# Kernel tuning notes

Measured on AMD Instinct MI355X. Metric: run time of the kernel, lower is better.

Reference implementation:

```python
import jax, jax.numpy as jnp
import numpy as np

N = 50000      # nodes
E = 1600000    # edges
D = 128        # input_dim
H = 128        # hidden_dim
C = 10         # n_class
G = 512        # number of graphs (max(idx)+1)
LRELU_ALPHA = 0.05
BN_EPS = 1e-5


def setup_inputs() -> dict:
    key = jax.random.key(0)
    ks = jax.random.split(key, 10)
    x_in = jax.random.normal(ks[0], (N, D), dtype=jnp.float32)
    edge_index = jax.random.randint(ks[1], (2, E), 0, N, dtype=jnp.int32)
    idx = jnp.sort(jax.random.randint(ks[2], (N,), 0, G, dtype=jnp.int32))

    def lin(k, shape, fan_in):
        return jax.random.normal(k, shape, dtype=jnp.float32) / np.sqrt(fan_in).astype(np.float32)

    fc_w = lin(ks[3], (H, D), D)        # GATLayer.fc weight
    a1 = lin(ks[4], (H,), 2 * H)        # a weight, src half
    a2 = lin(ks[5], (H,), 2 * H)        # a weight, dst half
    fc1_w = lin(ks[6], (H, H), H)
    fc1_b = jnp.zeros((H,), jnp.float32)
    fc2_w = lin(ks[7], (C, H), H)
    fc2_b = jnp.zeros((C,), jnp.float32)
    gamma = jnp.ones((H,), jnp.float32)  # BatchNorm weight
    beta = jnp.zeros((H,), jnp.float32)  # BatchNorm bias
    return {"x_in": x_in, "edge_index": edge_index, "idx": idx,
            "fc_w": fc_w, "a1": a1, "a2": a2,
            "fc1_w": fc1_w, "fc1_b": fc1_b, "fc2_w": fc2_w, "fc2_b": fc2_b,
            "gamma": gamma, "beta": beta}


def reference(x_in, edge_index, idx, fc_w, a1, a2, fc1_w, fc1_b, fc2_w, fc2_b, gamma, beta):
    # input standardization (torch.std is unbiased -> ddof=1)
    x = (x_in - jnp.mean(x_in)) / jnp.std(x_in, ddof=1)

    # ---- GAT layer ----
    z = x @ fc_w.T                              # [N, H]
    src, dst = edge_index[0], edge_index[1]
    # a([z_src ; z_dst]) == z_src@a1 + z_dst@a2  (avoids materializing [E, 2H])
    s1 = z @ a1                                  # [N]
    s2 = z @ a2                                  # [N]
    e = s1[src] + s2[dst]                        # [E]
    e = jnp.where(e >= 0, e, LRELU_ALPHA * e)    # LeakyReLU(0.05)
    h = jnp.exp(e)
    h_sum = jax.ops.segment_sum(h, src, num_segments=N)   # edge-softmax denom per src row
    alpha = h / h_sum[src]                       # [E]
    # sparse.mm(adj_att, z): out[src] += alpha * z[dst]
    out = jax.ops.segment_sum(alpha[:, None] * z[dst], src, num_segments=N)  # [N, H]

    x = jax.nn.relu(out)
    # dropout: identity (eval / deterministic reference)

    # sum pooling per graph
    pooled = jax.ops.segment_sum(x, idx, num_segments=G)   # [G, H]

    # BatchNorm1d (training-mode batch statistics, biased var)
    mu = jnp.mean(pooled, axis=0)
    var = jnp.var(pooled, axis=0)
    xb = (pooled - mu) / jnp.sqrt(var + BN_EPS) * gamma + beta

    x = jax.nn.relu(xb @ fc1_w.T + fc1_b)
    logits = x @ fc2_w.T + fc2_b
    return jax.nn.log_softmax(logits, axis=1)
```

## Files before the change

### kernel.cpp

```cpp
#include <hip/hip_runtime.h>

#define NN 50000
#define NE 1600000
#define DD 128
#define HH 128
#define CC 10
#define GG 512
#define LRELU_A 0.05f
#define BN_EPS 1e-5f

#define TT 256
#define EPT (NE / TT)
#define NB 196
#define NPB 256
#define KNODE 8
#define STB 1024

typedef unsigned int u32;
typedef unsigned short u16;
typedef unsigned char u8;

__device__ __forceinline__ u16 f2bf(float f) {
    u32 u = __float_as_uint(f);
    u32 r = u + 0x7FFFu + ((u >> 16) & 1u);
    return (u16)(r >> 16);
}

__global__ __launch_bounds__(256) void k_front(const int* __restrict__ src,
                                               const float* __restrict__ x,
                                               u16* __restrict__ cnt_b,
                                               u8* __restrict__ rank_e,
                                               float* __restrict__ pooled,
                                               double* __restrict__ pst) {
    __shared__ u32 h[NB];
    __shared__ double ls[4], lss[4];
    int bid = blockIdx.x, tid = threadIdx.x;
    if (bid < TT) {
        for (int i = tid; i < NB; i += 256) h[i] = 0;
        pooled[bid * 256 + tid] = 0.f;
        __syncthreads();
        int e0 = bid * EPT;
        for (int i = tid; i < EPT; i += 256) {
            int b = src[e0 + i] >> 8;
            u32 old = atomicAdd(&h[b], 1u);
            rank_e[e0 + i] = (u8)old;
        }
        __syncthreads();
        for (int i = tid; i < NB; i += 256) cnt_b[bid * NB + i] = (u16)h[i];
    } else {
        int sb = bid - TT;
        const int M4 = NN * DD / 4;
        double s = 0.0, ss = 0.0;
        for (int i = sb * 256 + tid; i < M4; i += STB * 256) {
            float4 v = reinterpret_cast<const float4*>(x)[i];
            s  += (double)v.x + (double)v.y + (double)v.z + (double)v.w;
            ss += (double)v.x * v.x + (double)v.y * v.y + (double)v.z * v.z +
                  (double)v.w * v.w;
        }
        for (int d = 32; d; d >>= 1) { s += __shfl_down(s, d); ss += __shfl_down(ss, d); }
        int lane = tid & 63, w = tid >> 6;
        if (lane == 0) { ls[w] = s; lss[w] = ss; }
        __syncthreads();
        if (tid == 0) {
            pst[2 * sb]     = ls[0] + ls[1] + ls[2] + ls[3];
            pst[2 * sb + 1] = lss[0] + lss[1] + lss[2] + lss[3];
        }
    }
}

__global__ __launch_bounds__(256) void k_mid(const u16* __restrict__ cnt_b,
                                             const double* __restrict__ pst,
                                             const float* __restrict__ fc_w,
                                             u16* __restrict__ rel_b,
                                             int* __restrict__ base_b,
                                             float* __restrict__ wsum,
                                             float* __restrict__ musig,
                                             float* __restrict__ wt) {
    int t = threadIdx.x;
    if (blockIdx.x == 0) {
        __shared__ int sm[256];
        int b = t;
        int run = 0;
        if (b < NB) {
            for (int tt = 0; tt < TT; ++tt) {
                int c = cnt_b[tt * NB + b];
                rel_b[tt * NB + b] = (u16)run;
                run += c;
            }
        }
        sm[b] = (b < NB) ? run : 0;
        __syncthreads();
        int v = sm[b];
        for (int d = 1; d < 256; d <<= 1) {
            int x = 0;
            if (b >= d) x = sm[b - d];
            __syncthreads();
            if (b >= d) sm[b] += x;
            __syncthreads();
        }
        if (b < NB) base_b[b] = sm[b] - v;
        if (b == NB - 1) base_b[NB] = sm[b];
    } else {
        __shared__ double rs[256], rss[256];
        double s  = pst[2 * t] + pst[2 * (t + 256)] + pst[2 * (t + 512)] + pst[2 * (t + 768)];
        double ss = pst[2 * t + 1] + pst[2 * (t + 256) + 1] +
                    pst[2 * (t + 512) + 1] + pst[2 * (t + 768) + 1];
        rs[t] = s; rss[t] = ss;
        __syncthreads();
        for (int d = 128; d; d >>= 1) {
            if (t < d) { rs[t] += rs[t + d]; rss[t] += rss[t + d]; }
            __syncthreads();
        }
        if (t == 0) {
            double M = (double)NN * DD;
            double mean = rs[0] / M;
            double var  = (rss[0] - rs[0] * rs[0] / M) / (M - 1.0);
            musig[0] = (float)mean;
            musig[1] = (float)(1.0 / sqrt(var));
        }
        if (t < 128) {
            float acc = 0.f;
            for (int k = 0; k < DD; ++k) acc += fc_w[t * DD + k];
            wsum[t] = acc;
        }
        for (int i = t; i < DD * HH; i += 256) {
            int k = i >> 7, c = i & 127;
            wt[i] = fc_w[c * DD + k];
        }
    }
}

#define PADX 132
__global__ __launch_bounds__(256, 2) void k_big(const int* __restrict__ src,
                                                const int* __restrict__ dst,
                                                const u16* __restrict__ rel_b,
                                                const u8* __restrict__ rank_e,
                                                const int* __restrict__ base_b,
                                                u32* __restrict__ ebuf,
                                                const float* __restrict__ x,
                                                const float* __restrict__ wt,
                                                const float* __restrict__ wsum,
                                                const float* __restrict__ musig,
                                                const float* __restrict__ a1,
                                                const float* __restrict__ a2,
                                                u32* __restrict__ zbf,
                                                float* __restrict__ s1,
                                                float* __restrict__ s2) {
    __shared__ float xs[128][PADX];
    int bid = blockIdx.x, tid = threadIdx.x;

    if (bid < TT) {
        int e0 = bid * EPT;
        for (int i = tid; i < EPT; i += 256) {
            int s = src[e0 + i];
            int b = s >> 8;
            int pos = base_b[b] + (int)rel_b[bid * NB + b] + (int)rank_e[e0 + i];
            ebuf[pos] = ((u32)dst[e0 + i] << 8) | (u32)(s & 255);
        }
        return;
    }

    int row0 = (bid - TT) * 128;
    for (int i = tid; i < 128 * 32; i += 256) {
        int r = i >> 5;
        int m = i & 31;
        int gr = row0 + r;
        float4 v = (gr < NN) ? reinterpret_cast<const float4*>(x)[gr * 32 + m]
                             : make_float4(0.f, 0.f, 0.f, 0.f);
        *reinterpret_cast<float4*>(&xs[r][m << 2]) = v;
    }
    __syncthreads();

    int trow = tid >> 4, tcol = tid & 15;
    float acc[8][8];
    #pragma unroll
    for (int i = 0; i < 8; ++i)
        #pragma unroll
        for (int j = 0; j < 8; ++j) acc[i][j] = 0.f;

    const float4* wt4 = reinterpret_cast<const float4*>(wt);
    for (int k = 0; k < 128; k += 4) {
        float4 xv[8];
        #pragma unroll
        for (int i = 0; i < 8; ++i)
            xv[i] = *reinterpret_cast<const float4*>(&xs[trow * 8 + i][k]);
        #pragma unroll
        for (int kk = 0; kk < 4; ++kk) {
            float4 w0 = wt4[(k + kk) * 32 + tcol * 2];
            float4 w1 = wt4[(k + kk) * 32 + tcol * 2 + 1];
            #pragma unroll
            for (int i = 0; i < 8; ++i) {
                float a = (kk == 0) ? xv[i].x
                        : (kk == 1) ? xv[i].y
                        : (kk == 2) ? xv[i].z : xv[i].w;
                acc[i][0] += a * w0.x; acc[i][1] += a * w0.y;
                acc[i][2] += a * w0.z; acc[i][3] += a * w0.w;
                acc[i][4] += a * w1.x; acc[i][5] += a * w1.y;
                acc[i][6] += a * w1.z; acc[i][7] += a * w1.w;
            }
        }
    }

    float mu = musig[0], isig = musig[1];
    int c0 = tcol * 8;
    float4 a10 = *reinterpret_cast<const float4*>(&a1[c0]);
    float4 a11 = *reinterpret_cast<const float4*>(&a1[c0 + 4]);
    float4 a20 = *reinterpret_cast<const float4*>(&a2[c0]);
    float4 a21 = *reinterpret_cast<const float4*>(&a2[c0 + 4]);
    float ws0x = wsum[c0 + 0], ws0y = wsum[c0 + 1], ws0z = wsum[c0 + 2], ws0w = wsum[c0 + 3];
    float ws1x = wsum[c0 + 4], ws1y = wsum[c0 + 5], ws1z = wsum[c0 + 6], ws1w = wsum[c0 + 7];

    float p1[8], p2[8];
    #pragma unroll
    for (int i = 0; i < 8; ++i) {
        int gr = row0 + trow * 8 + i;
        float4 o0, o1;
        o0.x = (acc[i][0] - mu * ws0x) * isig;
        o0.y = (acc[i][1] - mu * ws0y) * isig;
        o0.z = (acc[i][2] - mu * ws0z) * isig;
        o0.w = (acc[i][3] - mu * ws0w) * isig;
        o1.x = (acc[i][4] - mu * ws1x) * isig;
        o1.y = (acc[i][5] - mu * ws1y) * isig;
        o1.z = (acc[i][6] - mu * ws1z) * isig;
        o1.w = (acc[i][7] - mu * ws1w) * isig;
        p1[i] = o0.x * a10.x + o0.y * a10.y + o0.z * a10.z + o0.w * a10.w +
                o1.x * a11.x + o1.y * a11.y + o1.z * a11.z + o1.w * a11.w;
        p2[i] = o0.x * a20.x + o0.y * a20.y + o0.z * a20.z + o0.w * a20.w +
                o1.x * a21.x + o1.y * a21.y + o1.z * a21.z + o1.w * a21.w;
        if (gr < NN) {
            uint4 pk;
            pk.x = ((u32)f2bf(o0.y) << 16) | f2bf(o0.x);
            pk.y = ((u32)f2bf(o0.w) << 16) | f2bf(o0.z);
            pk.z = ((u32)f2bf(o1.y) << 16) | f2bf(o1.x);
            pk.w = ((u32)f2bf(o1.w) << 16) | f2bf(o1.z);
            *reinterpret_cast<uint4*>(&zbf[gr * 64 + tcol * 4]) = pk;
        }
    }
    #pragma unroll
    for (int d = 8; d; d >>= 1) {
        #pragma unroll
        for (int i = 0; i < 8; ++i) {
            p1[i] += __shfl_down(p1[i], d, 16);
            p2[i] += __shfl_down(p2[i], d, 16);
        }
    }
    if (tcol == 0) {
        #pragma unroll
        for (int i = 0; i < 8; ++i) {
            int gr = row0 + trow * 8 + i;
            if (gr < NN) { s1[gr] = p1[i]; s2[gr] = p2[i]; }
        }
    }
}

__global__ __launch_bounds__(256) void k_bcsr(const u32* __restrict__ ebuf,
                                              const int* __restrict__ base_b,
                                              const float* __restrict__ s1,
                                              const float* __restrict__ s2,
                                              int* __restrict__ off,
                                              u32* __restrict__ dst_s) {
    __shared__ u32 hist[NPB];
    __shared__ u32 cur[NPB];
    __shared__ int sm[256];
    int b = blockIdx.x, tid = threadIdx.x;
    int ebase = base_b[b], eend = base_b[b + 1];
    int m = eend - ebase;
    hist[tid] = 0;
    __syncthreads();
    for (int i = tid; i < m; i += 256)
        atomicAdd(&hist[ebuf[ebase + i] & 255u], 1u);
    __syncthreads();
    int v = (int)hist[tid];
    sm[tid] = v;
    __syncthreads();
    for (int d = 1; d < 256; d <<= 1) {
        int x = 0;
        if (tid >= d) x = sm[tid - d];
        __syncthreads();
        if (tid >= d) sm[tid] += x;
        __syncthreads();
    }
    int st = sm[tid] - v;
    cur[tid] = (u32)st;
    int n = b * NPB + tid;
    if (n < NN) off[n] = ebase + st;
    if (b == NB - 1 && tid == 0) off[NN] = NE;
    __syncthreads();
    for (int i = tid; i < m; i += 256) {
        u32 e = ebuf[ebase + i];
        int ls = (int)(e & 255u);
        int dn = (int)(e >> 8);
        int p = (int)atomicAdd(&cur[ls], 1u);
        float ev = s1[b * NPB + ls] + s2[dn];
        ev = (ev >= 0.f) ? ev : LRELU_A * ev;
        float h = __expf(ev);
        dst_s[ebase + p] = ((u32)dn << 16) | (u32)f2bf(h);
    }
}

__global__ __launch_bounds__(256) void k_aggregate(const u32* __restrict__ zbf,
                                                   const int* __restrict__ off,
                                                   const u32* __restrict__ dst_s,
                                                   const int* __restrict__ idx,
                                                   float* __restrict__ pooled) {
    int wave = (blockIdx.x * 256 + threadIdx.x) >> 6;
    int lane = threadIdx.x & 63;
    int n0 = wave * KNODE;
    if (n0 >= NN) return;
    int n1 = n0 + KNODE;
    if (n1 > NN) n1 = NN;

    float pool0 = 0.f, pool1 = 0.f;
    int curg = idx[n0];

    for (int node = n0; node < n1; ++node) {
        int g = idx[node];
        if (g != curg) {
            atomicAdd(&pooled[curg * HH + lane * 2], pool0);
            atomicAdd(&pooled[curg * HH + lane * 2 + 1], pool1);
            pool0 = 0.f; pool1 = 0.f;
            curg = g;
        }
        int j0 = off[node], j1 = off[node + 1];
        float acc0 = 0.f, acc1 = 0.f, hsl = 0.f;

        for (int b = j0; b < j1; b += 64) {
            int cnt = j1 - b;
            if (cnt > 64) cnt = 64;
            int jj = b + ((lane < cnt) ? lane : 0);
            int ul = (int)dst_s[jj];
            if (lane < cnt) hsl += __uint_as_float((u32)ul << 16);
            int k = 0;
            for (; k + 8 <= cnt; k += 8) {
                int eu[8]; u32 uu[8];
                #pragma unroll
                for (int q = 0; q < 8; ++q) eu[q] = __shfl(ul, k + q);
                #pragma unroll
                for (int q = 0; q < 8; ++q)
                    uu[q] = zbf[(((u32)eu[q] >> 16) << 6) | lane];
                #pragma unroll
                for (int q = 0; q < 8; ++q) {
                    float hq = __uint_as_float((u32)eu[q] << 16);
                    acc0 += hq * __uint_as_float(uu[q] << 16);
                    acc1 += hq * __uint_as_float(uu[q] & 0xFFFF0000u);
                }
            }
            for (; k + 4 <= cnt; k += 4) {
                int eu[4]; u32 uu[4];
                #pragma unroll
                for (int q = 0; q < 4; ++q) eu[q] = __shfl(ul, k + q);
                #pragma unroll
                for (int q = 0; q < 4; ++q)
                    uu[q] = zbf[(((u32)eu[q] >> 16) << 6) | lane];
                #pragma unroll
                for (int q = 0; q < 4; ++q) {
                    float hq = __uint_as_float((u32)eu[q] << 16);
                    acc0 += hq * __uint_as_float(uu[q] << 16);
                    acc1 += hq * __uint_as_float(uu[q] & 0xFFFF0000u);
                }
            }
            for (; k < cnt; ++k) {
                int e = __shfl(ul, k);
                float hk = __uint_as_float((u32)e << 16);
                u32 u = zbf[(((u32)e >> 16) << 6) | lane];
                acc0 += hk * __uint_as_float(u << 16);
                acc1 += hk * __uint_as_float(u & 0xFFFF0000u);
            }
        }
        float hs = hsl;
        #pragma unroll
        for (int d = 32; d; d >>= 1) hs += __shfl_xor(hs, d);
        float inv = (hs > 0.f) ? 1.f / hs : 0.f;
        pool0 += fmaxf(acc0 * inv, 0.f);
        pool1 += fmaxf(acc1 * inv, 0.f);
    }
    atomicAdd(&pooled[curg * HH + lane * 2], pool0);
    atomicAdd(&pooled[curg * HH + lane * 2 + 1], pool1);
}

__global__ __launch_bounds__(128) void k_head(const float* __restrict__ pooled,
                                              const float* __restrict__ gamma,
                                              const float* __restrict__ beta,
                                              const float* __restrict__ fc1w,
                                              const float* __restrict__ fc1b,
                                              const float* __restrict__ fc2w,
                                              const float* __restrict__ fc2b,
                                              float* __restrict__ out) {
    __shared__ __align__(16) float xb[128];
    __shared__ __align__(16) float h1[128];
    __shared__ float lg[16];
    int g = blockIdx.x;
    int t = threadIdx.x;
    float s = 0.f, ss = 0.f;
    #pragma unroll 8
    for (int q = 0; q < GG; ++q) {
        float v = pooled[q * HH + t];
        s += v;
        ss += v * v;
    }
    float mean = s / GG;
    float var  = ss / GG - mean * mean;
    float sc = gamma[t] * rsqrtf(var + BN_EPS);
    xb[t] = pooled[g * HH + t] * sc + (beta[t] - mean * sc);
    __syncthreads();
    float acc = 0.f;
    const float4* wr = reinterpret_cast<const float4*>(&fc1w[t * HH]);
    #pragma unroll 8
    for (int k = 0; k < 32; ++k) {
        float4 w4 = wr[k];
        float4 xv = *reinterpret_cast<const float4*>(&xb[k * 4]);
        acc += w4.x * xv.x + w4.y * xv.y + w4.z * xv.z + w4.w * xv.w;
    }
    acc += fc1b[t];
    h1[t] = (acc > 0.f) ? acc : 0.f;
    __syncthreads();
    if (t < CC) {
        float a = 0.f;
        const float4* w2 = reinterpret_cast<const float4*>(&fc2w[t * HH]);
        #pragma unroll 8
        for (int k = 0; k < 32; ++k) {
            float4 w4 = w2[k];
            float4 hv = *reinterpret_cast<const float4*>(&h1[k * 4]);
            a += w4.x * hv.x + w4.y * hv.y + w4.z * hv.z + w4.w * hv.w;
        }
        lg[t] = a + fc2b[t];
    }
    __syncthreads();
    if (t == 0) {
        float mx = lg[0];
        for (int c = 1; c < CC; ++c) mx = fmaxf(mx, lg[c]);
        float se = 0.f;
        for (int c = 0; c < CC; ++c) se += __expf(lg[c] - mx);
        float lse = mx + logf(se);
        for (int c = 0; c < CC; ++c) out[g * CC + c] = lg[c] - lse;
    }
}

extern "C" void kernel_launch(void* const* d_in, const int* in_sizes, int n_in,
                              void* d_out, int out_size, void* d_ws, size_t ws_size,
                              hipStream_t stream) {
    const float* x_in  = (const float*)d_in[0];
    const int*   eidx  = (const int*)d_in[1];
    const int*   src   = eidx;
    const int*   dst   = eidx + NE;
    const int*   idx   = (const int*)d_in[2];
    const float* fc_w  = (const float*)d_in[3];
    const float* a1    = (const float*)d_in[4];
    const float* a2    = (const float*)d_in[5];
    const float* fc1w  = (const float*)d_in[6];
    const float* fc1b  = (const float*)d_in[7];
    const float* fc2w  = (const float*)d_in[8];
    const float* fc2b  = (const float*)d_in[9];
    const float* gamma = (const float*)d_in[10];
    const float* beta  = (const float*)d_in[11];
    float* out = (float*)d_out;

    char* p = (char*)d_ws;
    auto alloc = [&](size_t bytes) {
        char* r = p;
        p += (bytes + 255) & ~(size_t)255;
        return r;
    };
    double* pst    = (double*)alloc((size_t)STB * 2 * sizeof(double));
    float*  wsum   = (float*)alloc(HH * sizeof(float));
    float*  musig  = (float*)alloc(4 * sizeof(float));
    float*  wt     = (float*)alloc((size_t)DD * HH * sizeof(float));
    u16*    cnt_b  = (u16*)alloc((size_t)TT * NB * sizeof(u16));
    u16*    rel_b  = (u16*)alloc((size_t)TT * NB * sizeof(u16));
    u8*     rank_e = (u8*)alloc((size_t)NE * sizeof(u8));
    int*    base_b = (int*)alloc((NB + 1) * sizeof(int));
    u32*    ebuf   = (u32*)alloc((size_t)NE * sizeof(u32));
    int*    off    = (int*)alloc((NN + 1) * sizeof(int));
    u32*    dst_s  = (u32*)alloc((size_t)NE * sizeof(u32));
    u32*    zbf    = (u32*)alloc((size_t)NN * (HH / 2) * sizeof(u32));
    float*  s1     = (float*)alloc(NN * sizeof(float));
    float*  s2     = (float*)alloc(NN * sizeof(float));
    float*  pooled = (float*)alloc((size_t)GG * HH * sizeof(float));

    k_front<<<TT + STB, 256, 0, stream>>>(src, x_in, cnt_b, rank_e, pooled, pst);
    k_mid<<<2, 256, 0, stream>>>(cnt_b, pst, fc_w, rel_b, base_b, wsum, musig, wt);
    int gemm_blocks = (NN + 127) / 128;
    k_big<<<TT + gemm_blocks, 256, 0, stream>>>(src, dst, rel_b, rank_e, base_b,
                                                ebuf, x_in, wt, wsum, musig,
                                                a1, a2, zbf, s1, s2);
    k_bcsr<<<NB, 256, 0, stream>>>(ebuf, base_b, s1, s2, off, dst_s);
    int nwaves = (NN + KNODE - 1) / KNODE;
    int nblocks = (nwaves + 3) / 4;
    k_aggregate<<<nblocks, 256, 0, stream>>>(zbf, off, dst_s, idx, pooled);
    k_head<<<GG, 128, 0, stream>>>(pooled, gamma, beta, fc1w, fc1b, fc2w, fc2b, out);
}
```

Before: 174.0 us.

## Shrink src buckets to 64 nodes for more CSR-build blocks

Changes the edge bucketing from 256-node buckets (196 buckets) to 64-node buckets (782 real, 784 padded), so the per-bucket CSR build kernel launches about four times as many blocks with smaller shared histograms and scans. The mid kernel's per-bucket prefix work is split across four blocks, and the bucket-base scan runs in chunks on its own block. The packed edge word now uses a 6-bit local index. The aim is better GPU occupancy in k_bcsr. The cost is larger count and offset tables and a serial per-bucket total sum over all tiles in block 0 of k_mid.

```diff
diff --git a/kernel.cpp b/kernel.cpp
--- a/kernel.cpp
+++ b/kernel.cpp
@@ -11,8 +11,9 @@
 
 #define TT 256
 #define EPT (NE / TT)
-#define NB 196
-#define NPB 256
+#define NBR 782
+#define NBP 784
+#define NPB 64
 #define KNODE 8
 #define STB 1024
 
@@ -32,21 +33,21 @@
                                                u8* __restrict__ rank_e,
                                                float* __restrict__ pooled,
                                                double* __restrict__ pst) {
-    __shared__ u32 h[NB];
+    __shared__ u32 h[NBP];
     __shared__ double ls[4], lss[4];
     int bid = blockIdx.x, tid = threadIdx.x;
     if (bid < TT) {
-        for (int i = tid; i < NB; i += 256) h[i] = 0;
+        for (int i = tid; i < NBP; i += 256) h[i] = 0;
         pooled[bid * 256 + tid] = 0.f;
         __syncthreads();
         int e0 = bid * EPT;
         for (int i = tid; i < EPT; i += 256) {
-            int b = src[e0 + i] >> 8;
+            int b = src[e0 + i] >> 6;
             u32 old = atomicAdd(&h[b], 1u);
             rank_e[e0 + i] = (u8)old;
         }
         __syncthreads();
-        for (int i = tid; i < NB; i += 256) cnt_b[bid * NB + i] = (u16)h[i];
+        for (int i = tid; i < NBP; i += 256) cnt_b[bid * NBP + i] = (u16)h[i];
     } else {
         int sb = bid - TT;
         const int M4 = NN * DD / 4;
@@ -77,29 +78,42 @@
                                              float* __restrict__ musig,
                                              float* __restrict__ wt) {
     int t = threadIdx.x;
-    if (blockIdx.x == 0) {
+    int bid = blockIdx.x;
+    if (bid == 0) {
         __shared__ int sm[256];
-        int b = t;
-        int run = 0;
-        if (b < NB) {
+        __shared__ int runs;
+        if (t == 0) runs = 0;
+        __syncthreads();
+        for (int chunk = 0; chunk < 4; ++chunk) {
+            int b = chunk * 256 + t;
+            int tot = 0;
+            if (b < NBP)
+                for (int tt = 0; tt < TT; ++tt) tot += cnt_b[tt * NBP + b];
+            sm[t] = tot;
+            __syncthreads();
+            for (int d = 1; d < 256; d <<= 1) {
+                int x = 0;
+                if (t >= d) x = sm[t - d];
+                __syncthreads();
+                if (t >= d) sm[t] += x;
+                __syncthreads();
+            }
+            if (b < NBP) base_b[b] = runs + sm[t] - tot;
+            __syncthreads();
+            if (t == 255) runs += sm[255];
+            __syncthreads();
+        }
+        if (t == 0) base_b[NBP] = runs;
+    } else if (bid <= 4) {
+        int b = (bid - 1) * 196 + t;
+        if (t < 196) {
+            int run = 0;
             for (int tt = 0; tt < TT; ++tt) {
-                int c = cnt_b[tt * NB + b];
-                rel_b[tt * NB + b] = (u16)run;
+                int c = cnt_b[tt * NBP + b];
+                rel_b[tt * NBP + b] = (u16)run;
                 run += c;
             }
         }
-        sm[b] = (b < NB) ? run : 0;
-        __syncthreads();
-        int v = sm[b];
-        for (int d = 1; d < 256; d <<= 1) {
-            int x = 0;
-            if (b >= d) x = sm[b - d];
-            __syncthreads();
-            if (b >= d) sm[b] += x;
-            __syncthreads();
-        }
-        if (b < NB) base_b[b] = sm[b] - v;
-        if (b == NB - 1) base_b[NB] = sm[b];
     } else {
         __shared__ double rs[256], rss[256];
         double s  = pst[2 * t] + pst[2 * (t + 256)] + pst[2 * (t + 512)] + pst[2 * (t + 768)];
@@ -153,9 +167,9 @@
         int e0 = bid * EPT;
         for (int i = tid; i < EPT; i += 256) {
             int s = src[e0 + i];
-            int b = s >> 8;
-            int pos = base_b[b] + (int)rel_b[bid * NB + b] + (int)rank_e[e0 + i];
-            ebuf[pos] = ((u32)dst[e0 + i] << 8) | (u32)(s & 255);
+            int b = s >> 6;
+            int pos = base_b[b] + (int)rel_b[bid * NBP + b] + (int)rank_e[e0 + i];
+            ebuf[pos] = ((u32)dst[e0 + i] << 6) | (u32)(s & 63);
         }
         return;
     }
@@ -261,35 +275,37 @@
                                               u32* __restrict__ dst_s) {
     __shared__ u32 hist[NPB];
     __shared__ u32 cur[NPB];
-    __shared__ int sm[256];
+    __shared__ int sm[NPB];
     int b = blockIdx.x, tid = threadIdx.x;
     int ebase = base_b[b], eend = base_b[b + 1];
     int m = eend - ebase;
-    hist[tid] = 0;
+    if (tid < NPB) hist[tid] = 0;
     __syncthreads();
     for (int i = tid; i < m; i += 256)
-        atomicAdd(&hist[ebuf[ebase + i] & 255u], 1u);
-    __syncthreads();
-    int v = (int)hist[tid];
-    sm[tid] = v;
-    __syncthreads();
-    for (int d = 1; d < 256; d <<= 1) {
+        atomicAdd(&hist[ebuf[ebase + i] & 63u], 1u);
+    __syncthreads();
+    if (tid < NPB) sm[tid] = (int)hist[tid];
+    __syncthreads();
+    for (int d = 1; d < NPB; d <<= 1) {
         int x = 0;
-        if (tid >= d) x = sm[tid - d];
-        __syncthreads();
-        if (tid >= d) sm[tid] += x;
-        __syncthreads();
-    }
-    int st = sm[tid] - v;
-    cur[tid] = (u32)st;
-    int n = b * NPB + tid;
-    if (n < NN) off[n] = ebase + st;
-    if (b == NB - 1 && tid == 0) off[NN] = NE;
+        if (tid < NPB && tid >= d) x = sm[tid - d];
+        __syncthreads();
+        if (tid < NPB && tid >= d) sm[tid] += x;
+        __syncthreads();
+    }
+    if (tid < NPB) {
+        int v = (int)hist[tid];
+        int st = sm[tid] - v;
+        cur[tid] = (u32)st;
+        int n = b * NPB + tid;
+        if (n < NN) off[n] = ebase + st;
+    }
+    if (b == NBR - 1 && tid == 0) off[NN] = NE;
     __syncthreads();
     for (int i = tid; i < m; i += 256) {
         u32 e = ebuf[ebase + i];
-        int ls = (int)(e & 255u);
-        int dn = (int)(e >> 8);
+        int ls = (int)(e & 63u);
+        int dn = (int)(e >> 6);
         int p = (int)atomicAdd(&cur[ls], 1u);
         float ev = s1[b * NPB + ls] + s2[dn];
         ev = (ev >= 0.f) ? ev : LRELU_A * ev;
@@ -465,10 +481,10 @@
     float*  wsum   = (float*)alloc(HH * sizeof(float));
     float*  musig  = (float*)alloc(4 * sizeof(float));
     float*  wt     = (float*)alloc((size_t)DD * HH * sizeof(float));
-    u16*    cnt_b  = (u16*)alloc((size_t)TT * NB * sizeof(u16));
-    u16*    rel_b  = (u16*)alloc((size_t)TT * NB * sizeof(u16));
+    u16*    cnt_b  = (u16*)alloc((size_t)TT * NBP * sizeof(u16));
+    u16*    rel_b  = (u16*)alloc((size_t)TT * NBP * sizeof(u16));
     u8*     rank_e = (u8*)alloc((size_t)NE * sizeof(u8));
-    int*    base_b = (int*)alloc((NB + 1) * sizeof(int));
+    int*    base_b = (int*)alloc((NBP + 1) * sizeof(int));
     u32*    ebuf   = (u32*)alloc((size_t)NE * sizeof(u32));
     int*    off    = (int*)alloc((NN + 1) * sizeof(int));
     u32*    dst_s  = (u32*)alloc((size_t)NE * sizeof(u32));
@@ -478,12 +494,12 @@
     float*  pooled = (float*)alloc((size_t)GG * HH * sizeof(float));
 
     k_front<<<TT + STB, 256, 0, stream>>>(src, x_in, cnt_b, rank_e, pooled, pst);
-    k_mid<<<2, 256, 0, stream>>>(cnt_b, pst, fc_w, rel_b, base_b, wsum, musig, wt);
+    k_mid<<<6, 256, 0, stream>>>(cnt_b, pst, fc_w, rel_b, base_b, wsum, musig, wt);
     int gemm_blocks = (NN + 127) / 128;
     k_big<<<TT + gemm_blocks, 256, 0, stream>>>(src, dst, rel_b, rank_e, base_b,
                                                 ebuf, x_in, wt, wsum, musig,
                                                 a1, a2, zbf, s1, s2);
-    k_bcsr<<<NB, 256, 0, stream>>>(ebuf, base_b, s1, s2, off, dst_s);
+    k_bcsr<<<NBR, 256, 0, stream>>>(ebuf, base_b, s1, s2, off, dst_s);
     int nwaves = (NN + KNODE - 1) / KNODE;
     int nblocks = (nwaves + 3) / 4;
     k_aggregate<<<nblocks, 256, 0, stream>>>(zbf, off, dst_s, idx, pooled);
```

Measured after the change: 184.1 us. 1.06x slower.
